# Kernel optimization log

Hardware: AMD Instinct MI355X
Metric: run time of the kernel (lower is better)

## Reference

```python
import jax, jax.numpy as jnp
import numpy as np

NUM_CLASSES = 1000
FEAT_DIM = 256
N = 262144
ALPHA = 0.5


def setup_inputs() -> dict:
    key = jax.random.key(0)
    k1, k2, k3 = jax.random.split(key, 3)
    x = jax.random.normal(k1, (N, FEAT_DIM), dtype=jnp.float32)
    labels = jax.random.randint(k2, (N,), 0, NUM_CLASSES, dtype=jnp.int64)
    centers = jax.random.normal(k3, (NUM_CLASSES, FEAT_DIM), dtype=jnp.float32)
    return {"x": x, "labels": labels, "centers": centers}


def reference(x, labels, centers):
    # loss: mean euclidean distance to own class center, halved
    centers_batch = centers[labels]                      # [N, D] gather
    dist = jnp.sqrt(jnp.sum((x - centers_batch) ** 2, axis=1))  # [N]
    loss = dist.mean() / 2.0

    # center update (torch.no_grad block): single-pass segment mean
    C = centers.shape[0]
    sums = jax.ops.segment_sum(x, labels, num_segments=C)           # [C, D]
    counts = jax.ops.segment_sum(jnp.ones((x.shape[0],), x.dtype), labels,
                                 num_segments=C)                     # [C]
    # mean(x[mask] - center_i) = mean(x[mask]) - center_i
    mean_x = sums / jnp.maximum(counts, 1.0)[:, None]
    delta = mean_x - centers
    new_centers = jnp.where(counts[:, None] > 0,
                            centers + ALPHA * delta, centers)
    return loss, new_centers
```

## Files before the change

### kernel.cpp

```cpp
#include <hip/hip_runtime.h>
#include <math.h>


#define D 256
#define SETUP_BLOCKS 64
#define SETUP_THREADS 1024
#define MAIN_THREADS 256
#define CH 128
#define CPB 2

__device__ __forceinline__ void grid_barrier(int* bar) {
    __syncthreads();
    if (threadIdx.x == 0) {
        __threadfence();
        atomicAdd(bar, 1);
        while (__hip_atomic_load(bar, __ATOMIC_ACQUIRE, __HIP_MEMORY_SCOPE_AGENT)
               < SETUP_BLOCKS) {
            __builtin_amdgcn_s_sleep(2);
        }
    }
    __syncthreads();
}

__global__ __launch_bounds__(256) void init_kernel(float* __restrict__ accum,
                                                   int* __restrict__ counts,
                                                   int* __restrict__ bars,
                                                   double* __restrict__ lossacc) {
    float4* a4 = (float4*)accum;
    for (int i = blockIdx.x * 256 + threadIdx.x; i < 64000; i += gridDim.x * 256)
        a4[i] = make_float4(0.f, 0.f, 0.f, 0.f);
    if (blockIdx.x == 0) {
        for (int i = threadIdx.x; i < 1024; i += 256) counts[i] = 0;
        if (threadIdx.x < 3) bars[threadIdx.x] = 0;
        if (threadIdx.x == 0) *lossacc = 0.0;
    }
}

__global__ __launch_bounds__(SETUP_THREADS) void setup_kernel(
        const int* __restrict__ lraw, int n,
        int* __restrict__ counts, int* __restrict__ offsets,
        int* __restrict__ bar0, int* __restrict__ bar1,
        int* __restrict__ hist_all, int* __restrict__ rowidx) {
    __shared__ int sh[1024];
    __shared__ int s_flag;
    const int tid = threadIdx.x;
    const int b = blockIdx.x;

    if (tid == 0) s_flag = 0;
    sh[tid] = 0;
    __syncthreads();
    if (tid < 512 && 2 * tid + 1 < n) {
        if (lraw[2 * tid + 1]) atomicOr(&s_flag, 1);
    }
    __syncthreads();
    const int f64 = (s_flag == 0) ? 1 : 0;

    for (int i = b * SETUP_THREADS + tid; i < n; i += SETUP_BLOCKS * SETUP_THREADS) {
        const int lbl = f64 ? lraw[2 * (size_t)i] : lraw[i];
        atomicAdd(&sh[lbl], 1);
    }
    __syncthreads();
    const int myh = sh[tid];
    hist_all[b * 1024 + tid] = myh;
    if (myh) atomicAdd(&counts[tid], myh);

    grid_barrier(bar0);

    if (b == 0) {
        const int v = counts[tid];
        sh[tid] = v;
        __syncthreads();
        for (int off = 1; off < 1024; off <<= 1) {
            const int add = (tid >= off) ? sh[tid - off] : 0;
            __syncthreads();
            sh[tid] += add;
            __syncthreads();
        }
        offsets[tid] = sh[tid] - v;
    }

    grid_barrier(bar1);

    int base = offsets[tid];
    for (int pb = 0; pb < b; ++pb) base += hist_all[pb * 1024 + tid];
    __syncthreads();
    sh[tid] = base;
    __syncthreads();
    for (int i = b * SETUP_THREADS + tid; i < n; i += SETUP_BLOCKS * SETUP_THREADS) {
        const int lbl = f64 ? lraw[2 * (size_t)i] : lraw[i];
        const int pos = atomicAdd(&sh[lbl], 1);
        rowidx[pos] = i;
    }
}

__global__ __launch_bounds__(MAIN_THREADS) void main_kernel(
        const float* __restrict__ x, const float* __restrict__ centers,
        const int* __restrict__ offsets, const int* __restrict__ counts,
        const int* __restrict__ rowidx,
        float* __restrict__ accum, double* __restrict__ lossacc) {
    const int c = blockIdx.x / CPB;
    const int p = blockIdx.x % CPB;
    const int tid = threadIdx.x;
    const int wave = tid >> 6;
    const int lane = tid & 63;

    __shared__ float s_sum[4][D];
    __shared__ float s_loss[4];

    const float4 ctr = ((const float4*)(centers + (size_t)c * D))[lane];
    const int start = offsets[c];
    const int cnt = counts[c];

    float4 sum = make_float4(0.f, 0.f, 0.f, 0.f);
    float lsum = 0.f;

    for (int cb = p * CH; cb < cnt; cb += CPB * CH) {
        const int len = min(CH, cnt - cb);
        const int lo = start + cb;
        const int i0 = (lane < len) ? rowidx[lo + lane] : 0;
        const int i1 = (64 + lane < len) ? rowidx[lo + 64 + lane] : 0;
        const int nw = (len > wave) ? ((len - wave + 3) >> 2) : 0;

        constexpr int U = 8;
        float4 A[U], B[U];

        auto LOADB = [&](int bb, float4* buf) -> int {
            int nv = nw - bb * U;
            nv = nv < 0 ? 0 : (nv > U ? U : nv);
            #pragma unroll
            for (int k = 0; k < U; ++k) {
                if (k < nv) {
                    const int pos = wave + 4 * (bb * U + k);
                    const int r = __shfl(pos < 64 ? i0 : i1, pos & 63, 64);
                    buf[k] = ((const float4*)(x + (size_t)r * D))[lane];
                }
            }
            return nv;
        };
        auto PROC = [&](const float4* buf, int nv) {
            #pragma unroll
            for (int k = 0; k < U; ++k) {
                if (k < nv) {
                    const float4 v = buf[k];
                    sum.x += v.x; sum.y += v.y; sum.z += v.z; sum.w += v.w;
                    const float dx = v.x - ctr.x, dy = v.y - ctr.y;
                    const float dz = v.z - ctr.z, dw = v.w - ctr.w;
                    float sq = dx * dx + dy * dy + dz * dz + dw * dw;
                    #pragma unroll
                    for (int o = 32; o; o >>= 1) sq += __shfl_xor(sq, o, 64);
                    lsum += sqrtf(sq);
                }
            }
        };

        int bb = 0;
        int nA = LOADB(0, A);
        while (nA) {
            const int nB = LOADB(bb + 1, B);
            PROC(A, nA);
            if (!nB) break;
            nA = LOADB(bb + 2, A);
            PROC(B, nB);
            bb += 2;
        }
    }

    ((float4*)&s_sum[wave][lane * 4])[0] = sum;
    if (lane == 0) s_loss[wave] = lsum;
    __syncthreads();

    const float tot = s_sum[0][tid] + s_sum[1][tid] + s_sum[2][tid] + s_sum[3][tid];
    atomicAdd(&accum[(size_t)c * D + tid], tot);
    if (tid == 0) {
        const double bl = (double)(s_loss[0] + s_loss[1] + s_loss[2] + s_loss[3]);
        atomicAdd(lossacc, bl);
    }
}

__global__ __launch_bounds__(256) void finalize_kernel(
        const float* __restrict__ accum, const float* __restrict__ centers,
        const int* __restrict__ counts, const double* __restrict__ lossacc,
        int n, float* __restrict__ out) {
    const int c = blockIdx.x;
    const int t = threadIdx.x;
    const int cnt = counts[c];
    const float cs = centers[(size_t)c * D + t];
    const float s = accum[(size_t)c * D + t];
    const float o = (cnt > 0) ? cs + 0.5f * (s / (float)cnt - cs) : cs;
    out[1 + (size_t)c * D + t] = o;
    if (c == 0 && t == 0) out[0] = (float)(*lossacc / (double)n * 0.5);
}

extern "C" void kernel_launch(void* const* d_in, const int* in_sizes, int n_in,
                              void* d_out, int out_size, void* d_ws, size_t ws_size,
                              hipStream_t stream) {
    const float* x       = (const float*)d_in[0];
    const int*   lraw    = (const int*)d_in[1];
    const float* centers = (const float*)d_in[2];
    float* out = (float*)d_out;

    const int n = in_sizes[1];
    const int C = in_sizes[2] / D;

    char* ws = (char*)d_ws;
    int*    counts   = (int*)(ws + 0);
    int*    offsets  = (int*)(ws + 4096);
    int*    bars     = (int*)(ws + 8192);
    double* lossacc  = (double*)(ws + 8208);
    int*    hist_all = (int*)(ws + 16384);
    int*    rowidx   = (int*)(ws + 524288);
    float*  accum    = (float*)(ws + 2097152);

    hipLaunchKernelGGL(init_kernel, dim3(128), dim3(256), 0, stream,
                       accum, counts, bars, lossacc);
    hipLaunchKernelGGL(setup_kernel, dim3(SETUP_BLOCKS), dim3(SETUP_THREADS), 0, stream,
                       lraw, n, counts, offsets, &bars[0], &bars[1], hist_all, rowidx);
    hipLaunchKernelGGL(main_kernel, dim3(C * CPB), dim3(MAIN_THREADS), 0, stream,
                       x, centers, offsets, counts, rowidx, accum, lossacc);
    hipLaunchKernelGGL(finalize_kernel, dim3(C), dim3(256), 0, stream,
                       accum, centers, counts, lossacc, n, out);
}
```

Measured before the change: 421.2 us.

## Stage row indices in LDS and use branchless contiguous-half row loads

Each block now takes a contiguous half of its class's rows instead of interleaved 128-row chunks. Row indices are staged through shared memory 256 at a time. Loads and processing become unconditional, with out-of-range rows clamped to row 0 and masked by a zero weight, so the loop has no per-element branches and the double buffer always stays full. This removes divergent predication and shuffle-based index broadcast, but it wastes loads on the padded tail of each batch and adds block-level syncs per segment.

```diff
diff --git a/kernel.cpp b/kernel.cpp
--- a/kernel.cpp
+++ b/kernel.cpp
@@ -5,9 +5,8 @@
 #define D 256
 #define SETUP_BLOCKS 64
 #define SETUP_THREADS 1024
-#define MAIN_THREADS 256
-#define CH 128
-#define CPB 2
+#define U 8
+#define BROWS 32
 
 __device__ __forceinline__ void grid_barrier(int* bar) {
     __syncthreads();
@@ -93,75 +92,76 @@
     }
 }
 
-__global__ __launch_bounds__(MAIN_THREADS) void main_kernel(
+__global__ __launch_bounds__(256, 4) void main_kernel(
         const float* __restrict__ x, const float* __restrict__ centers,
         const int* __restrict__ offsets, const int* __restrict__ counts,
         const int* __restrict__ rowidx,
         float* __restrict__ accum, double* __restrict__ lossacc) {
-    const int c = blockIdx.x / CPB;
-    const int p = blockIdx.x % CPB;
+    const int c = blockIdx.x >> 1;
+    const int p = blockIdx.x & 1;
     const int tid = threadIdx.x;
     const int wave = tid >> 6;
     const int lane = tid & 63;
 
+    __shared__ int s_idx[256];
     __shared__ float s_sum[4][D];
     __shared__ float s_loss[4];
 
     const float4 ctr = ((const float4*)(centers + (size_t)c * D))[lane];
     const int start = offsets[c];
     const int cnt = counts[c];
+    const int half = (cnt + 1) >> 1;
+    const int lo = start + p * half;
+    int len = cnt - p * half;
+    len = len < 0 ? 0 : (len > half ? half : len);
 
     float4 sum = make_float4(0.f, 0.f, 0.f, 0.f);
     float lsum = 0.f;
 
-    for (int cb = p * CH; cb < cnt; cb += CPB * CH) {
-        const int len = min(CH, cnt - cb);
-        const int lo = start + cb;
-        const int i0 = (lane < len) ? rowidx[lo + lane] : 0;
-        const int i1 = (64 + lane < len) ? rowidx[lo + 64 + lane] : 0;
-        const int nw = (len > wave) ? ((len - wave + 3) >> 2) : 0;
-
-        constexpr int U = 8;
+    for (int seg0 = 0; seg0 < len; seg0 += 256) {
+        const int seg = min(256, len - seg0);
+        __syncthreads();
+        if (tid < seg) s_idx[tid] = rowidx[lo + seg0 + tid];
+        __syncthreads();
+
+        const int nb = (seg + BROWS - 1) / BROWS;
+
         float4 A[U], B[U];
 
-        auto LOADB = [&](int bb, float4* buf) -> int {
-            int nv = nw - bb * U;
-            nv = nv < 0 ? 0 : (nv > U ? U : nv);
+        auto LOADB = [&](int bb, float4* buf) {
             #pragma unroll
             for (int k = 0; k < U; ++k) {
-                if (k < nv) {
-                    const int pos = wave + 4 * (bb * U + k);
-                    const int r = __shfl(pos < 64 ? i0 : i1, pos & 63, 64);
-                    buf[k] = ((const float4*)(x + (size_t)r * D))[lane];
-                }
+                const int pos = bb * BROWS + wave * U + k;
+                const int safe = (pos < seg) ? pos : 0;
+                const int r = s_idx[safe];
+                buf[k] = ((const float4*)(x + (size_t)r * D))[lane];
             }
-            return nv;
         };
-        auto PROC = [&](const float4* buf, int nv) {
+        auto PROCB = [&](int bb, const float4* buf) {
             #pragma unroll
             for (int k = 0; k < U; ++k) {
-                if (k < nv) {
-                    const float4 v = buf[k];
-                    sum.x += v.x; sum.y += v.y; sum.z += v.z; sum.w += v.w;
-                    const float dx = v.x - ctr.x, dy = v.y - ctr.y;
-                    const float dz = v.z - ctr.z, dw = v.w - ctr.w;
-                    float sq = dx * dx + dy * dy + dz * dz + dw * dw;
-                    #pragma unroll
-                    for (int o = 32; o; o >>= 1) sq += __shfl_xor(sq, o, 64);
-                    lsum += sqrtf(sq);
-                }
+                const int pos = bb * BROWS + wave * U + k;
+                const float w = (pos < seg) ? 1.f : 0.f;
+                const float4 v = buf[k];
+                sum.x = fmaf(w, v.x, sum.x);
+                sum.y = fmaf(w, v.y, sum.y);
+                sum.z = fmaf(w, v.z, sum.z);
+                sum.w = fmaf(w, v.w, sum.w);
+                const float dx = v.x - ctr.x, dy = v.y - ctr.y;
+                const float dz = v.z - ctr.z, dw = v.w - ctr.w;
+                float sq = w * (dx * dx + dy * dy + dz * dz + dw * dw);
+                #pragma unroll
+                for (int o = 32; o; o >>= 1) sq += __shfl_xor(sq, o, 64);
+                lsum += sqrtf(sq);
             }
         };
 
-        int bb = 0;
-        int nA = LOADB(0, A);
-        while (nA) {
-            const int nB = LOADB(bb + 1, B);
-            PROC(A, nA);
-            if (!nB) break;
-            nA = LOADB(bb + 2, A);
-            PROC(B, nB);
-            bb += 2;
+        LOADB(0, A);
+        for (int bb = 0; bb < nb; bb += 2) {
+            LOADB(bb + 1, B);
+            PROCB(bb, A);
+            LOADB(bb + 2, A);
+            PROCB(bb + 1, B);
         }
     }
 
@@ -215,7 +215,7 @@
                        accum, counts, bars, lossacc);
     hipLaunchKernelGGL(setup_kernel, dim3(SETUP_BLOCKS), dim3(SETUP_THREADS), 0, stream,
                        lraw, n, counts, offsets, &bars[0], &bars[1], hist_all, rowidx);
-    hipLaunchKernelGGL(main_kernel, dim3(C * CPB), dim3(MAIN_THREADS), 0, stream,
+    hipLaunchKernelGGL(main_kernel, dim3(C * 2), dim3(256), 0, stream,
                        x, centers, offsets, counts, rowidx, accum, lossacc);
     hipLaunchKernelGGL(finalize_kernel, dim3(C), dim3(256), 0, stream,
                        accum, centers, counts, lossacc, n, out);
```

Result: faster. 403.0 us (-4.3%).
